# Performance work log

Hardware: AMD Instinct MI355X
Metric: run time of the kernel (lower is better)

Reference implementation:

```python
import jax, jax.numpy as jnp
import numpy as np

NUM_E_BITS = 5
NUM_M_BITS = 10
EXP_BIAS = 2 ** (NUM_E_BITS - 1) - 1  # 15


def float2bit(f):
    """Faithful vectorized port of torch float2bit (num_e_bits=5, num_m_bits=10).

    Only the first NUM_M_BITS mantissa bits are computed (the torch code computes
    127 and slices [..., :num_m_bits]; the sliced-away bits never affect output).
    """
    dt = f.dtype
    is_nan = jnp.isnan(f)
    is_inf = jnp.isinf(f)
    is_neg_inf = is_inf & (f < 0)
    is_pos_inf = is_inf & (f > 0)
    is_normal = ~(is_nan | is_inf)

    fsafe = jnp.where(is_normal, f, jnp.asarray(1.0, dt))  # avoid nan/inf math
    # sign bit: (sign(v + 0.001) * -1 + 1) * 0.5
    s = (jnp.sign(fsafe + 0.001) * -1.0 + 1.0) * 0.5
    f1 = jnp.abs(fsafe)
    e_sci = jnp.floor(jnp.log2(f1))
    # log2(0) -> -inf gets clamped to -(2^(E-1)-1)
    e_sci = jnp.where(jnp.isneginf(e_sci), jnp.asarray(-float(EXP_BIAS), dt), e_sci)
    e_dec = e_sci + EXP_BIAS

    # integer2bit: bits k = floor(e_dec / 2^k) % 2 for k = E-1 .. 0
    e_pows = (2.0 ** jnp.arange(NUM_E_BITS - 1, -1, -1)).astype(dt)  # [16,8,4,2,1]
    e_bits = jnp.mod(jnp.floor(e_dec[..., None] / e_pows), 2.0)

    f2 = f1 / (2.0 ** e_sci)
    r = jnp.mod(f2, 1.0)
    m_pows = (2.0 ** jnp.arange(NUM_M_BITS)).astype(dt)
    m_bits = jnp.floor(2.0 * jnp.mod(r[..., None] * m_pows, 1.0))

    bits = jnp.concatenate([s[..., None], e_bits, m_bits], axis=-1)  # [..., 16]

    # special-value patterns
    z1 = jnp.zeros((1,), dt)
    o1 = jnp.ones((1,), dt)
    oe = jnp.ones((NUM_E_BITS,), dt)
    zm = jnp.zeros((NUM_M_BITS,), dt)
    nan_pat = jnp.concatenate([z1, oe, o1, jnp.zeros((NUM_M_BITS - 1,), dt)])
    pinf_pat = jnp.concatenate([z1, oe, zm])
    ninf_pat = jnp.concatenate([o1, oe, zm])
    bits = jnp.where(is_nan[..., None], nan_pat, bits)
    bits = jnp.where(is_pos_inf[..., None], pinf_pat, bits)
    bits = jnp.where(is_neg_inf[..., None], ninf_pat, bits)
    return bits


def setup_inputs() -> dict:
    key = jax.random.key(0)
    x = jax.random.normal(key, (256, 2048, 4), dtype=jnp.float32)
    return {"x": x}


def reference(x):
    bits = float2bit(x)  # [B, S, input_size, 16]
    out = bits.reshape(*bits.shape[:-2], bits.shape[-2] * bits.shape[-1])
    return (out - 0.5) * 2.0
```

## Files before the change

### kernel.cpp

```cpp
#include <hip/hip_runtime.h>


typedef float vfloat4 __attribute__((ext_vector_type(4)));

__global__ __launch_bounds__(256) void preencoder_f2b_kernel(
    const float* __restrict__ x, vfloat4* __restrict__ out, int n4) {
  const int stride = gridDim.x * blockDim.x;
  for (int t = blockIdx.x * blockDim.x + threadIdx.x; t < n4; t += stride) {
    int i = t >> 2;
    int c = t & 3;

    float f = x[i];
    unsigned u = __float_as_uint(f);
    unsigned a = u & 0x7FFFFFFFu;

    unsigned w;
    bool sign_half = false;

    if (a > 0x7F800000u) {
      w = 0x7E00u;
    } else if (a == 0x7F800000u) {
      w = (u >> 31) ? 0xFC00u : 0x7C00u;
    } else {
      if (a == 0u) {
        w = 0u;
      } else {
        int e8 = (int)(a >> 23);
        int E;
        unsigned mant;
        if (e8 != 0) {
          E = e8 - 127;
          mant = a & 0x7FFFFFu;
        } else {
          int p = 31 - __clz((int)a);
          E = p - 149;
          mant = (a << (23 - p)) & 0x7FFFFFu;
        }
        w = ((unsigned)((E + 15) & 31) << 10) | (mant >> 13);
      }
      float tt = f + 0.001f;
      if (tt < 0.0f) {
        w |= 0x8000u;
      } else if (tt == 0.0f) {
        sign_half = true;
      }
    }

    int hi = 15 - 4 * c;
    vfloat4 o;
    o.x = ((w >> hi) & 1u) ? 1.0f : -1.0f;
    o.y = ((w >> (hi - 1)) & 1u) ? 1.0f : -1.0f;
    o.z = ((w >> (hi - 2)) & 1u) ? 1.0f : -1.0f;
    o.w = ((w >> (hi - 3)) & 1u) ? 1.0f : -1.0f;
    if (c == 0 && sign_half) o.x = 0.0f;

    out[t] = o;
  }
}

extern "C" void kernel_launch(void* const* d_in, const int* in_sizes, int n_in,
                              void* d_out, int out_size, void* d_ws, size_t ws_size,
                              hipStream_t stream) {
  const float* x = (const float*)d_in[0];
  vfloat4* out = (vfloat4*)d_out;
  int n4 = out_size / 4;
  int threads = 256;
  int blocks = 2048;
  preencoder_f2b_kernel<<<blocks, threads, 0, stream>>>(x, out, n4);
}
```

Measured before the change: 143.1 us.

## Unroll grid-stride loop with prefetched loads and cheaper half-conversion bit decode

When the output size is exactly sixteen times the thread count, the grid-stride loop becomes a fixed four-round unrolled schedule. Each round handles four input elements and loads the next round's values early, so more memory requests are in flight per thread. The common normal-range case now truncates the mantissa and uses the hardware float-to-half conversion instead of the branchy exponent and mantissa extraction. Output signs are built with XOR bit tricks instead of selects. The gains depend on the exact size match, and the fast path's range check and sign-zero handling must stay bit-exact with the reference.

```diff
diff --git a/kernel.cpp b/kernel.cpp
--- a/kernel.cpp
+++ b/kernel.cpp
@@ -1,60 +1,90 @@
 #include <hip/hip_runtime.h>
+#include <hip/hip_fp16.h>
 
 
 typedef float vfloat4 __attribute__((ext_vector_type(4)));
 
+__device__ __forceinline__ unsigned decode_w(float f) {
+  unsigned u = __float_as_uint(f);
+  unsigned a = u & 0x7FFFFFFFu;
+  unsigned w;
+  if (__builtin_expect(a - 0x38800000u < 0x0F000000u, 1)) {
+    float tm = __uint_as_float(a & 0xFFFFE000u);
+    w = (unsigned)__half_as_ushort(__float2half(tm));
+  } else if (a > 0x7F800000u) {
+    w = 0x7E00u;
+  } else if (a == 0x7F800000u) {
+    w = 0x7C00u;
+  } else if (a == 0u) {
+    w = 0u;
+  } else {
+    int e8 = (int)(a >> 23);
+    int E; unsigned mant;
+    if (e8 != 0) {
+      E = e8 - 127;
+      mant = a & 0x7FFFFFu;
+    } else {
+      int p = 31 - __clz((int)a);
+      E = p - 149;
+      mant = (a << (23 - p)) & 0x7FFFFFu;
+    }
+    w = ((unsigned)((E + 15) & 31) << 10) | (mant >> 13);
+  }
+  float tt = f + 0.001f;
+  if (tt < 0.0f) w |= 0x8000u;
+  return w;
+}
+
+__device__ __forceinline__ vfloat4 extract4(unsigned w, int sh, bool szero) {
+  unsigned nib = w >> sh;
+  vfloat4 o;
+  o.x = __uint_as_float(0xBF800000u ^ ((nib << 28) & 0x80000000u));
+  o.y = __uint_as_float(0xBF800000u ^ ((nib << 29) & 0x80000000u));
+  o.z = __uint_as_float(0xBF800000u ^ ((nib << 30) & 0x80000000u));
+  o.w = __uint_as_float(0xBF800000u ^ (nib << 31));
+  if (szero) o.x = 0.0f;
+  return o;
+}
+
 __global__ __launch_bounds__(256) void preencoder_f2b_kernel(
     const float* __restrict__ x, vfloat4* __restrict__ out, int n4) {
-  const int stride = gridDim.x * blockDim.x;
-  for (int t = blockIdx.x * blockDim.x + threadIdx.x; t < n4; t += stride) {
-    int i = t >> 2;
-    int c = t & 3;
+  const int S = gridDim.x * blockDim.x;
+  const int tid = blockIdx.x * blockDim.x + threadIdx.x;
+  const int c = tid & 3;
+  const int sh = 12 - 4 * c;
 
-    float f = x[i];
-    unsigned u = __float_as_uint(f);
-    unsigned a = u & 0x7FFFFFFFu;
+  if (n4 == 16 * S) {
+    const int S4 = S >> 2;
+    int t = tid;
+    int e = tid >> 2;
+    float f[4];
+#pragma unroll
+    for (int j = 0; j < 4; ++j) f[j] = x[e + j * S4];
 
-    unsigned w;
-    bool sign_half = false;
-
-    if (a > 0x7F800000u) {
-      w = 0x7E00u;
-    } else if (a == 0x7F800000u) {
-      w = (u >> 31) ? 0xFC00u : 0x7C00u;
-    } else {
-      if (a == 0u) {
-        w = 0u;
-      } else {
-        int e8 = (int)(a >> 23);
-        int E;
-        unsigned mant;
-        if (e8 != 0) {
-          E = e8 - 127;
-          mant = a & 0x7FFFFFu;
-        } else {
-          int p = 31 - __clz((int)a);
-          E = p - 149;
-          mant = (a << (23 - p)) & 0x7FFFFFu;
-        }
-        w = ((unsigned)((E + 15) & 31) << 10) | (mant >> 13);
+#pragma unroll
+    for (int r = 0; r < 4; ++r) {
+      float g[4] = {0.0f, 0.0f, 0.0f, 0.0f};
+      if (r < 3) {
+        int en = e + S;
+#pragma unroll
+        for (int j = 0; j < 4; ++j) g[j] = x[en + j * S4];
       }
-      float tt = f + 0.001f;
-      if (tt < 0.0f) {
-        w |= 0x8000u;
-      } else if (tt == 0.0f) {
-        sign_half = true;
+#pragma unroll
+      for (int j = 0; j < 4; ++j) {
+        bool szero = (c == 0) && (f[j] == -0.001f);
+        out[t + j * S] = extract4(decode_w(f[j]), sh, szero);
       }
+#pragma unroll
+      for (int j = 0; j < 4; ++j) f[j] = g[j];
+      e += S;
+      t += 4 * S;
     }
-
-    int hi = 15 - 4 * c;
-    vfloat4 o;
-    o.x = ((w >> hi) & 1u) ? 1.0f : -1.0f;
-    o.y = ((w >> (hi - 1)) & 1u) ? 1.0f : -1.0f;
-    o.z = ((w >> (hi - 2)) & 1u) ? 1.0f : -1.0f;
-    o.w = ((w >> (hi - 3)) & 1u) ? 1.0f : -1.0f;
-    if (c == 0 && sign_half) o.x = 0.0f;
-
-    out[t] = o;
+  } else {
+    for (int t = tid; t < n4; t += S) {
+      int cc = t & 3;
+      bool szero = (cc == 0) && (x[t >> 2] == -0.001f);
+      out[t] = extract4(decode_w(x[t >> 2]), 12 - 4 * cc, szero);
+    }
   }
 }
 
```

New measurement: 141.1 us. About the same (-1.4%).
